# Kernel optimization log

Measured on AMD Instinct MI355X. Metric: run time of the kernel, lower is better.

The kernel has to match this reference:

```python
import jax, jax.numpy as jnp
import numpy as np

B, N, DIN, DOUT, H = 4, 2048, 512, 512, 8
HD = DOUT // H


def setup_inputs() -> dict:
    key = jax.random.key(0)
    ks = jax.random.split(key, 8)
    x = jax.random.normal(ks[0], (B, N, DIN), dtype=jnp.float32)
    mask = jax.random.randint(ks[1], (B, 1, N, N), 0, 2, dtype=jnp.int32)
    s = 1.0 / np.sqrt(DIN)
    Wq = jax.random.uniform(ks[2], (DOUT, DIN), jnp.float32, -s, s)
    Wk = jax.random.uniform(ks[3], (DOUT, DIN), jnp.float32, -s, s)
    Wv = jax.random.uniform(ks[4], (DOUT, DIN), jnp.float32, -s, s)
    bq = jax.random.uniform(ks[5], (DOUT,), jnp.float32, -s, s)
    bk = jax.random.uniform(ks[6], (DOUT,), jnp.float32, -s, s)
    bv = jax.random.uniform(ks[7], (DOUT,), jnp.float32, -s, s)
    return {"x": x, "Wq": Wq, "bq": bq, "Wk": Wk, "bk": bk, "Wv": Wv, "bv": bv, "mask": mask}


def reference(x, Wq, bq, Wk, bk, Wv, bv, mask):
    b, n, _ = x.shape
    # torch Linear: y = x @ W.T + b ; split heads -> [b, h, n, hd]
    def proj(W, bias):
        y = jnp.einsum('bnd,od->bno', x, W) + bias
        return y.reshape(b, n, H, HD).transpose(0, 2, 1, 3)
    Q, K, V = proj(Wq, bq), proj(Wk, bk), proj(Wv, bv)
    scores = jnp.einsum('bhnd,bhmd->bhnm', Q, K) / np.sqrt(HD).astype(np.float32)
    scores = jnp.where(mask == 0, jnp.float32(-1e9), scores)
    attn = jax.nn.softmax(scores, axis=-1)
    ctx = jnp.einsum('bhnm,bhmd->bhnd', attn, V)
    ctx = ctx.transpose(0, 2, 1, 3).reshape(b, n, DOUT)
    return jax.nn.elu(ctx)
```

## Files before the change

### kernel.cpp

```cpp
#include <hip/hip_runtime.h>
#include <math.h>
#include <stdint.h>

#define CB 4
#define CN 2048
#define CDIN 512
#define CDOUT 512
#define CH 8
#define CHD 64
#define CM (CB * CN)
#define CBH (CB * CH)
#define NKT (CN / 64)

typedef _Float16 f16x8 __attribute__((ext_vector_type(8)));
typedef _Float16 f16x4 __attribute__((ext_vector_type(4)));
typedef float    f32x4 __attribute__((ext_vector_type(4)));

#define QSCALE 0.1803368801111204f

__global__ __launch_bounds__(256) void cvt_kernel(
    const float* __restrict__ s0, _Float16* __restrict__ d0, int n0,
    const float* __restrict__ s1, _Float16* __restrict__ d1, int n1,
    const float* __restrict__ s2, _Float16* __restrict__ d2, int n2,
    const float* __restrict__ s3, _Float16* __restrict__ d3, int n3)
{
    const float* s; _Float16* d; int n;
    if (blockIdx.y == 0)      { s = s0; d = d0; n = n0; }
    else if (blockIdx.y == 1) { s = s1; d = d1; n = n1; }
    else if (blockIdx.y == 2) { s = s2; d = d2; n = n2; }
    else                      { s = s3; d = d3; n = n3; }
    int i = (blockIdx.x * 256 + threadIdx.x) * 8;
    const int stride = gridDim.x * 256 * 8;
    for (; i < n; i += stride) {
        float4 a = *(const float4*)&s[i];
        float4 b = *(const float4*)&s[i + 4];
        f16x8 h = {(_Float16)a.x, (_Float16)a.y, (_Float16)a.z, (_Float16)a.w,
                   (_Float16)b.x, (_Float16)b.y, (_Float16)b.z, (_Float16)b.w};
        *(f16x8*)&d[i] = h;
    }
}

__global__ __launch_bounds__(256) void maskbits_kernel(
    const int* __restrict__ mask, unsigned long long* __restrict__ mbits)
{
    const int idx = blockIdx.x * 256 + threadIdx.x;
    const int* src = mask + (size_t)idx * 64;
    unsigned long long m = 0;
    #pragma unroll
    for (int c = 0; c < 16; ++c) {
        int4 v = *(const int4*)&src[c * 4];
        unsigned long long bits = (v.x ? 1ull : 0ull) | (v.y ? 2ull : 0ull) |
                                  (v.z ? 4ull : 0ull) | (v.w ? 8ull : 0ull);
        m |= bits << (c * 4);
    }
    mbits[idx] = m;
}

__global__ __launch_bounds__(256) void proj_kernel(
    const _Float16* __restrict__ xh,
    const _Float16* __restrict__ Wqh, const float* __restrict__ bq,
    const _Float16* __restrict__ Wkh, const float* __restrict__ bk,
    const _Float16* __restrict__ Wvh, const float* __restrict__ bv,
    _Float16* __restrict__ Qf, _Float16* __restrict__ Kf, _Float16* __restrict__ Vt)
{
    const int z = blockIdx.z;
    const _Float16* W; const float* bias;
    if (z == 0)      { W = Wqh; bias = bq; }
    else if (z == 1) { W = Wkh; bias = bk; }
    else             { W = Wvh; bias = bv; }

    __shared__ _Float16 Xs[128][72];
    __shared__ _Float16 Ws[128][72];

    const int tid  = threadIdx.x;
    const int m0   = blockIdx.x * 128;
    const int o0   = blockIdx.y * 128;
    const int lane = tid & 63, w = tid >> 6;
    const int il   = lane & 15, quad = lane >> 4;

    f32x4 acc[2][8] = {};

    for (int k0 = 0; k0 < CDIN; k0 += 64) {
        #pragma unroll
        for (int i = 0; i < 4; ++i) {
            int seg = tid + i * 256;
            int row = seg >> 3, kc = (seg & 7) * 8;
            *(f16x8*)&Xs[row][kc] = *(const f16x8*)&xh[(size_t)(m0 + row) * CDIN + k0 + kc];
            *(f16x8*)&Ws[row][kc] = *(const f16x8*)&W[(size_t)(o0 + row) * CDIN + k0 + kc];
        }
        __syncthreads();
        #pragma unroll
        for (int dh = 0; dh < 2; ++dh) {
            f16x8 A0 = *(const f16x8*)&Xs[w * 32 + il][dh * 32 + quad * 8];
            f16x8 A1 = *(const f16x8*)&Xs[w * 32 + 16 + il][dh * 32 + quad * 8];
            #pragma unroll
            for (int s = 0; s < 8; ++s) {
                f16x8 Bv = *(const f16x8*)&Ws[s * 16 + il][dh * 32 + quad * 8];
                acc[0][s] = __builtin_amdgcn_mfma_f32_16x16x32_f16(A0, Bv, acc[0][s], 0, 0, 0);
                acc[1][s] = __builtin_amdgcn_mfma_f32_16x16x32_f16(A1, Bv, acc[1][s], 0, 0, 0);
            }
        }
        __syncthreads();
    }

    const int b  = m0 / CN;
    const int nb = m0 & (CN - 1);
    #pragma unroll
    for (int s = 0; s < 8; ++s) {
        const int o  = o0 + s * 16 + il;
        const int h  = o >> 6, d = o & 63;
        const int bh = b * CH + h;
        const float bval = bias[o];
        if (z < 2) {
            _Float16* dst = (z == 0) ? Qf : Kf;
            const float sc = (z == 0) ? QSCALE : 1.0f;
            #pragma unroll
            for (int mi = 0; mi < 2; ++mi) {
                #pragma unroll
                for (int r = 0; r < 4; ++r) {
                    int n = nb + w * 32 + mi * 16 + quad * 4 + r;
                    dst[((size_t)bh * CN + n) * CHD + d] =
                        (_Float16)((acc[mi][s][r] + bval) * sc);
                }
            }
        } else {
            #pragma unroll
            for (int mi = 0; mi < 2; ++mi) {
                int n0 = nb + w * 32 + mi * 16 + quad * 4;
                f16x4 pv = {(_Float16)(acc[mi][s][0] + bval),
                            (_Float16)(acc[mi][s][1] + bval),
                            (_Float16)(acc[mi][s][2] + bval),
                            (_Float16)(acc[mi][s][3] + bval)};
                *(f16x4*)&Vt[((size_t)bh * CHD + d) * CN + n0] = pv;
            }
        }
    }
}

__global__ __launch_bounds__(256) void attn_kernel(
    const _Float16* __restrict__ Qf, const _Float16* __restrict__ Kf,
    const _Float16* __restrict__ Vt, const unsigned long long* __restrict__ mbits,
    float* __restrict__ out)
{
    __shared__ _Float16 Ks[2][64][72];
    __shared__ _Float16 Vs[2][64][72];
    __shared__ _Float16 Ps[4][16][72];

    const int tid  = threadIdx.x;
    const int q0   = blockIdx.x * 64;
    const int bh   = blockIdx.y;
    const int b    = bh >> 3, h = bh & 7;
    const int lane = tid & 63, w = tid >> 6;
    const int il   = lane & 15, quad = lane >> 4;
    const int srow = tid >> 2, sc0 = (tid & 3) * 16;

    const _Float16* Qb = Qf + (size_t)bh * CN * CHD;
    const _Float16* Kb = Kf + (size_t)bh * CN * CHD;
    const _Float16* Vb = Vt + (size_t)bh * CHD * CN;

    const int qg = q0 + w * 16 + il;
    const unsigned long long* mrow = mbits + ((size_t)b * CN + qg) * NKT;

    f16x8 Qa0 = *(const f16x8*)&Qb[(size_t)qg * CHD + quad * 8];
    f16x8 Qa1 = *(const f16x8*)&Qb[(size_t)qg * CHD + 32 + quad * 8];

    const f16x8 ones = {1.f16, 1.f16, 1.f16, 1.f16, 1.f16, 1.f16, 1.f16, 1.f16};

    f32x4 oacc[4] = {};
    f32x4 lacc = {};

    uint4 kA, kB, vA, vB; unsigned long long mn;
    {
        const _Float16* kp = &Kb[(size_t)srow * CHD + sc0];
        const _Float16* vp = &Vb[(size_t)srow * CN + sc0];
        kA = *(const uint4*)kp; kB = *(const uint4*)(kp + 8);
        vA = *(const uint4*)vp; vB = *(const uint4*)(vp + 8);
        mn = mrow[0];
    }
    *(uint4*)&Ks[0][srow][sc0] = kA; *(uint4*)&Ks[0][srow][sc0 + 8] = kB;
    *(uint4*)&Vs[0][srow][sc0] = vA; *(uint4*)&Vs[0][srow][sc0 + 8] = vB;
    __syncthreads();

    for (int kt = 0; kt < NKT; ++kt) {
        const int cur = kt & 1;
        const unsigned long long mcur = mn;

        if (kt < NKT - 1) {
            const _Float16* kp = &Kb[(size_t)((kt + 1) * 64 + srow) * CHD + sc0];
            const _Float16* vp = &Vb[(size_t)srow * CN + (kt + 1) * 64 + sc0];
            kA = *(const uint4*)kp; kB = *(const uint4*)(kp + 8);
            vA = *(const uint4*)vp; vB = *(const uint4*)(vp + 8);
            mn = mrow[kt + 1];
        }

        f32x4 st[4] = {};
        #pragma unroll
        for (int s = 0; s < 4; ++s) {
            f16x8 A0 = *(const f16x8*)&Ks[cur][s * 16 + il][quad * 8];
            f16x8 A1 = *(const f16x8*)&Ks[cur][s * 16 + il][32 + quad * 8];
            st[s] = __builtin_amdgcn_mfma_f32_16x16x32_f16(A0, Qa0, st[s], 0, 0, 0);
            st[s] = __builtin_amdgcn_mfma_f32_16x16x32_f16(A1, Qa1, st[s], 0, 0, 0);
        }

        const uint32_t mlo = (uint32_t)mcur, mhi = (uint32_t)(mcur >> 32);
        #pragma unroll
        for (int s = 0; s < 4; ++s) {
            const uint32_t mm = (s < 2) ? mlo : mhi;
            const int base = (s & 1) * 16 + quad * 4;
            f16x4 pv;
            #pragma unroll
            for (int r = 0; r < 4; ++r) {
                float sv = ((mm >> (base + r)) & 1u) ? st[s][r] : -1e9f;
                pv[r] = (_Float16)__builtin_amdgcn_exp2f(sv);
            }
            *(f16x4*)&Ps[w][il][s * 16 + quad * 4] = pv;
        }

        f16x8 Pa0 = *(const f16x8*)&Ps[w][il][quad * 8];
        f16x8 Pa1 = *(const f16x8*)&Ps[w][il][32 + quad * 8];
        #pragma unroll
        for (int s = 0; s < 4; ++s) {
            f16x8 B0 = *(const f16x8*)&Vs[cur][s * 16 + il][quad * 8];
            f16x8 B1 = *(const f16x8*)&Vs[cur][s * 16 + il][32 + quad * 8];
            oacc[s] = __builtin_amdgcn_mfma_f32_16x16x32_f16(Pa0, B0, oacc[s], 0, 0, 0);
            oacc[s] = __builtin_amdgcn_mfma_f32_16x16x32_f16(Pa1, B1, oacc[s], 0, 0, 0);
        }
        lacc = __builtin_amdgcn_mfma_f32_16x16x32_f16(Pa0, ones, lacc, 0, 0, 0);
        lacc = __builtin_amdgcn_mfma_f32_16x16x32_f16(Pa1, ones, lacc, 0, 0, 0);

        if (kt < NKT - 1) {
            *(uint4*)&Ks[cur ^ 1][srow][sc0] = kA;
            *(uint4*)&Ks[cur ^ 1][srow][sc0 + 8] = kB;
            *(uint4*)&Vs[cur ^ 1][srow][sc0] = vA;
            *(uint4*)&Vs[cur ^ 1][srow][sc0 + 8] = vB;
            __syncthreads();
        }
    }

    #pragma unroll
    for (int s = 0; s < 4; ++s) {
        const int d = h * CHD + s * 16 + il;
        #pragma unroll
        for (int r = 0; r < 4; ++r) {
            int n = q0 + w * 16 + quad * 4 + r;
            float c = oacc[s][r] / lacc[r];
            out[((size_t)b * CN + n) * CDOUT + d] = c > 0.f ? c : expm1f(c);
        }
    }
}

extern "C" void kernel_launch(void* const* d_in, const int* in_sizes, int n_in,
                              void* d_out, int out_size, void* d_ws, size_t ws_size,
                              hipStream_t stream) {
    const float* x    = (const float*)d_in[0];
    const float* Wq   = (const float*)d_in[1];
    const float* bq   = (const float*)d_in[2];
    const float* Wk   = (const float*)d_in[3];
    const float* bk   = (const float*)d_in[4];
    const float* Wv   = (const float*)d_in[5];
    const float* bv   = (const float*)d_in[6];
    const int*   mask = (const int*)d_in[7];
    float* out = (float*)d_out;

    const size_t nx = (size_t)CM * CDIN;
    const size_t nw = (size_t)CDOUT * CDIN;
    const size_t nt = (size_t)CBH * CN * CHD;
    _Float16* xh  = (_Float16*)d_ws;
    _Float16* wqh = xh + nx;
    _Float16* wkh = wqh + nw;
    _Float16* wvh = wkh + nw;
    _Float16* Qf  = wvh + nw;
    _Float16* Kf  = Qf + nt;
    _Float16* Vt  = Kf + nt;
    unsigned long long* mbits = (unsigned long long*)(Vt + nt);

    cvt_kernel<<<dim3(2048, 4), 256, 0, stream>>>(
        x, xh, (int)nx, Wq, wqh, (int)nw, Wk, wkh, (int)nw, Wv, wvh, (int)nw);
    maskbits_kernel<<<dim3(CB * CN * NKT / 256), 256, 0, stream>>>(mask, mbits);
    proj_kernel<<<dim3(CM / 128, CDOUT / 128, 3), 256, 0, stream>>>(
        xh, wqh, bq, wkh, bk, wvh, bv, Qf, Kf, Vt);
    attn_kernel<<<dim3(CN / 64, CBH), 256, 0, stream>>>(
        Qf, Kf, Vt, mbits, out);
}
```

Baseline: 230.5 us.

## Double query rows per attention block and prefetch projection tiles into registers

The attention kernel now handles 128 query rows per block, two 16-row groups per wave, so each K/V tile staged in shared memory is reused twice as much and K/V global traffic is halved. The projection GEMM now loads the next k-slice into registers while the MFMAs for the current slice run, hiding global load latency. The cost is higher register pressure in both kernels and half as many attention blocks (512), which may reduce occupancy.

```diff
diff --git a/kernel.cpp b/kernel.cpp
--- a/kernel.cpp
+++ b/kernel.cpp
@@ -77,18 +77,33 @@
     const int o0   = blockIdx.y * 128;
     const int lane = tid & 63, w = tid >> 6;
     const int il   = lane & 15, quad = lane >> 4;
+    const int srow = tid >> 3, kc = (tid & 7) * 8;
 
     f32x4 acc[2][8] = {};
+    f16x8 xr[4], wr[4];
+
+    #pragma unroll
+    for (int i = 0; i < 4; ++i) {
+        xr[i] = *(const f16x8*)&xh[(size_t)(m0 + srow + i * 32) * CDIN + kc];
+        wr[i] = *(const f16x8*)&W[(size_t)(o0 + srow + i * 32) * CDIN + kc];
+    }
 
     for (int k0 = 0; k0 < CDIN; k0 += 64) {
         #pragma unroll
         for (int i = 0; i < 4; ++i) {
-            int seg = tid + i * 256;
-            int row = seg >> 3, kc = (seg & 7) * 8;
-            *(f16x8*)&Xs[row][kc] = *(const f16x8*)&xh[(size_t)(m0 + row) * CDIN + k0 + kc];
-            *(f16x8*)&Ws[row][kc] = *(const f16x8*)&W[(size_t)(o0 + row) * CDIN + k0 + kc];
+            *(f16x8*)&Xs[srow + i * 32][kc] = xr[i];
+            *(f16x8*)&Ws[srow + i * 32][kc] = wr[i];
         }
         __syncthreads();
+
+        if (k0 + 64 < CDIN) {
+            #pragma unroll
+            for (int i = 0; i < 4; ++i) {
+                xr[i] = *(const f16x8*)&xh[(size_t)(m0 + srow + i * 32) * CDIN + k0 + 64 + kc];
+                wr[i] = *(const f16x8*)&W[(size_t)(o0 + srow + i * 32) * CDIN + k0 + 64 + kc];
+            }
+        }
+
         #pragma unroll
         for (int dh = 0; dh < 2; ++dh) {
             f16x8 A0 = *(const f16x8*)&Xs[w * 32 + il][dh * 32 + quad * 8];
@@ -144,10 +159,10 @@
 {
     __shared__ _Float16 Ks[2][64][72];
     __shared__ _Float16 Vs[2][64][72];
-    __shared__ _Float16 Ps[4][16][72];
+    __shared__ _Float16 Ps[4][32][72];
 
     const int tid  = threadIdx.x;
-    const int q0   = blockIdx.x * 64;
+    const int q0   = blockIdx.x * 128;
     const int bh   = blockIdx.y;
     const int b    = bh >> 3, h = bh & 7;
     const int lane = tid & 63, w = tid >> 6;
@@ -158,24 +173,28 @@
     const _Float16* Kb = Kf + (size_t)bh * CN * CHD;
     const _Float16* Vb = Vt + (size_t)bh * CHD * CN;
 
-    const int qg = q0 + w * 16 + il;
-    const unsigned long long* mrow = mbits + ((size_t)b * CN + qg) * NKT;
-
-    f16x8 Qa0 = *(const f16x8*)&Qb[(size_t)qg * CHD + quad * 8];
-    f16x8 Qa1 = *(const f16x8*)&Qb[(size_t)qg * CHD + 32 + quad * 8];
+    const int qg0 = q0 + w * 32 + il;
+    const int qg1 = qg0 + 16;
+    const unsigned long long* mrow0 = mbits + ((size_t)b * CN + qg0) * NKT;
+    const unsigned long long* mrow1 = mbits + ((size_t)b * CN + qg1) * NKT;
+
+    f16x8 Qa0 = *(const f16x8*)&Qb[(size_t)qg0 * CHD + quad * 8];
+    f16x8 Qa1 = *(const f16x8*)&Qb[(size_t)qg0 * CHD + 32 + quad * 8];
+    f16x8 Qa2 = *(const f16x8*)&Qb[(size_t)qg1 * CHD + quad * 8];
+    f16x8 Qa3 = *(const f16x8*)&Qb[(size_t)qg1 * CHD + 32 + quad * 8];
 
     const f16x8 ones = {1.f16, 1.f16, 1.f16, 1.f16, 1.f16, 1.f16, 1.f16, 1.f16};
 
-    f32x4 oacc[4] = {};
-    f32x4 lacc = {};
-
-    uint4 kA, kB, vA, vB; unsigned long long mn;
+    f32x4 oacc0[4] = {}, oacc1[4] = {};
+    f32x4 lacc0 = {}, lacc1 = {};
+
+    uint4 kA, kB, vA, vB; unsigned long long mn0, mn1;
     {
         const _Float16* kp = &Kb[(size_t)srow * CHD + sc0];
         const _Float16* vp = &Vb[(size_t)srow * CN + sc0];
         kA = *(const uint4*)kp; kB = *(const uint4*)(kp + 8);
         vA = *(const uint4*)vp; vB = *(const uint4*)(vp + 8);
-        mn = mrow[0];
+        mn0 = mrow0[0]; mn1 = mrow1[0];
     }
     *(uint4*)&Ks[0][srow][sc0] = kA; *(uint4*)&Ks[0][srow][sc0 + 8] = kB;
     *(uint4*)&Vs[0][srow][sc0] = vA; *(uint4*)&Vs[0][srow][sc0 + 8] = vB;
@@ -183,50 +202,63 @@
 
     for (int kt = 0; kt < NKT; ++kt) {
         const int cur = kt & 1;
-        const unsigned long long mcur = mn;
+        const unsigned long long mc0 = mn0, mc1 = mn1;
 
         if (kt < NKT - 1) {
             const _Float16* kp = &Kb[(size_t)((kt + 1) * 64 + srow) * CHD + sc0];
             const _Float16* vp = &Vb[(size_t)srow * CN + (kt + 1) * 64 + sc0];
             kA = *(const uint4*)kp; kB = *(const uint4*)(kp + 8);
             vA = *(const uint4*)vp; vB = *(const uint4*)(vp + 8);
-            mn = mrow[kt + 1];
-        }
-
-        f32x4 st[4] = {};
+            mn0 = mrow0[kt + 1]; mn1 = mrow1[kt + 1];
+        }
+
+        f32x4 st0[4] = {}, st1[4] = {};
         #pragma unroll
         for (int s = 0; s < 4; ++s) {
             f16x8 A0 = *(const f16x8*)&Ks[cur][s * 16 + il][quad * 8];
             f16x8 A1 = *(const f16x8*)&Ks[cur][s * 16 + il][32 + quad * 8];
-            st[s] = __builtin_amdgcn_mfma_f32_16x16x32_f16(A0, Qa0, st[s], 0, 0, 0);
-            st[s] = __builtin_amdgcn_mfma_f32_16x16x32_f16(A1, Qa1, st[s], 0, 0, 0);
-        }
-
-        const uint32_t mlo = (uint32_t)mcur, mhi = (uint32_t)(mcur >> 32);
+            st0[s] = __builtin_amdgcn_mfma_f32_16x16x32_f16(A0, Qa0, st0[s], 0, 0, 0);
+            st0[s] = __builtin_amdgcn_mfma_f32_16x16x32_f16(A1, Qa1, st0[s], 0, 0, 0);
+            st1[s] = __builtin_amdgcn_mfma_f32_16x16x32_f16(A0, Qa2, st1[s], 0, 0, 0);
+            st1[s] = __builtin_amdgcn_mfma_f32_16x16x32_f16(A1, Qa3, st1[s], 0, 0, 0);
+        }
+
+        const uint32_t m0lo = (uint32_t)mc0, m0hi = (uint32_t)(mc0 >> 32);
+        const uint32_t m1lo = (uint32_t)mc1, m1hi = (uint32_t)(mc1 >> 32);
         #pragma unroll
         for (int s = 0; s < 4; ++s) {
-            const uint32_t mm = (s < 2) ? mlo : mhi;
+            const uint32_t mm0 = (s < 2) ? m0lo : m0hi;
+            const uint32_t mm1 = (s < 2) ? m1lo : m1hi;
             const int base = (s & 1) * 16 + quad * 4;
-            f16x4 pv;
+            f16x4 p0, p1;
             #pragma unroll
             for (int r = 0; r < 4; ++r) {
-                float sv = ((mm >> (base + r)) & 1u) ? st[s][r] : -1e9f;
-                pv[r] = (_Float16)__builtin_amdgcn_exp2f(sv);
-            }
-            *(f16x4*)&Ps[w][il][s * 16 + quad * 4] = pv;
-        }
-
-        f16x8 Pa0 = *(const f16x8*)&Ps[w][il][quad * 8];
-        f16x8 Pa1 = *(const f16x8*)&Ps[w][il][32 + quad * 8];
+                float s0v = ((mm0 >> (base + r)) & 1u) ? st0[s][r] : -1e9f;
+                float s1v = ((mm1 >> (base + r)) & 1u) ? st1[s][r] : -1e9f;
+                p0[r] = (_Float16)__builtin_amdgcn_exp2f(s0v);
+                p1[r] = (_Float16)__builtin_amdgcn_exp2f(s1v);
+            }
+            *(f16x4*)&Ps[w][il][s * 16 + quad * 4]      = p0;
+            *(f16x4*)&Ps[w][16 + il][s * 16 + quad * 4] = p1;
+        }
+
+        f16x8 Pa00 = *(const f16x8*)&Ps[w][il][quad * 8];
+        f16x8 Pa01 = *(const f16x8*)&Ps[w][il][32 + quad * 8];
+        f16x8 Pa10 = *(const f16x8*)&Ps[w][16 + il][quad * 8];
+        f16x8 Pa11 = *(const f16x8*)&Ps[w][16 + il][32 + quad * 8];
         #pragma unroll
         for (int s = 0; s < 4; ++s) {
             f16x8 B0 = *(const f16x8*)&Vs[cur][s * 16 + il][quad * 8];
             f16x8 B1 = *(const f16x8*)&Vs[cur][s * 16 + il][32 + quad * 8];
-            oacc[s] = __builtin_amdgcn_mfma_f32_16x16x32_f16(Pa0, B0, oacc[s], 0, 0, 0);
-            oacc[s] = __builtin_amdgcn_mfma_f32_16x16x32_f16(Pa1, B1, oacc[s], 0, 0, 0);
-        }
-        lacc = __builtin_amdgcn_mfma_f32_16x16x32_f16(Pa0, ones, lacc, 0, 0, 0);
-        lacc = __builtin_amdgcn_mfma_f32_16x16x32_f16(Pa1, ones, lacc, 0, 0, 0);
+            oacc0[s] = __builtin_amdgcn_mfma_f32_16x16x32_f16(Pa00, B0, oacc0[s], 0, 0, 0);
+            oacc0[s] = __builtin_amdgcn_mfma_f32_16x16x32_f16(Pa01, B1, oacc0[s], 0, 0, 0);
+            oacc1[s] = __builtin_amdgcn_mfma_f32_16x16x32_f16(Pa10, B0, oacc1[s], 0, 0, 0);
+            oacc1[s] = __builtin_amdgcn_mfma_f32_16x16x32_f16(Pa11, B1, oacc1[s], 0, 0, 0);
+        }
+        lacc0 = __builtin_amdgcn_mfma_f32_16x16x32_f16(Pa00, ones, lacc0, 0, 0, 0);
+        lacc0 = __builtin_amdgcn_mfma_f32_16x16x32_f16(Pa01, ones, lacc0, 0, 0, 0);
+        lacc1 = __builtin_amdgcn_mfma_f32_16x16x32_f16(Pa10, ones, lacc1, 0, 0, 0);
+        lacc1 = __builtin_amdgcn_mfma_f32_16x16x32_f16(Pa11, ones, lacc1, 0, 0, 0);
 
         if (kt < NKT - 1) {
             *(uint4*)&Ks[cur ^ 1][srow][sc0] = kA;
@@ -242,9 +274,12 @@
         const int d = h * CHD + s * 16 + il;
         #pragma unroll
         for (int r = 0; r < 4; ++r) {
-            int n = q0 + w * 16 + quad * 4 + r;
-            float c = oacc[s][r] / lacc[r];
-            out[((size_t)b * CN + n) * CDOUT + d] = c > 0.f ? c : expm1f(c);
+            int n0 = q0 + w * 32 + quad * 4 + r;
+            float c0 = oacc0[s][r] / lacc0[r];
+            out[((size_t)b * CN + n0) * CDOUT + d] = c0 > 0.f ? c0 : expm1f(c0);
+            int n1 = n0 + 16;
+            float c1 = oacc1[s][r] / lacc1[r];
+            out[((size_t)b * CN + n1) * CDOUT + d] = c1 > 0.f ? c1 : expm1f(c1);
         }
     }
 }
@@ -279,6 +314,6 @@
     maskbits_kernel<<<dim3(CB * CN * NKT / 256), 256, 0, stream>>>(mask, mbits);
     proj_kernel<<<dim3(CM / 128, CDOUT / 128, 3), 256, 0, stream>>>(
         xh, wqh, bq, wkh, bk, wvh, bv, Qf, Kf, Vt);
-    attn_kernel<<<dim3(CN / 64, CBH), 256, 0, stream>>>(
+    attn_kernel<<<dim3(CN / 128, CBH), 256, 0, stream>>>(
         Qf, Kf, Vt, mbits, out);
 }
```

Result: faster. 224.7 us (-2.5%).
